# Performance work log

Measured on AMD Instinct MI355X. Metric: run time of the kernel, lower is better.

Reference implementation:

```python
import jax, jax.numpy as jnp
import numpy as np

N = 100000      # nodes
E = 1600000     # edges
IN_FEATS = 256
HID = 64
N_LAYERS = 3
OUT_FEATS = 32


def _glorot(key, shape):
    lim = np.sqrt(6.0 / (shape[0] + shape[1]))
    return jax.random.uniform(key, shape, jnp.float32, -lim, lim)


def setup_inputs() -> dict:
    key = jax.random.key(0)
    ks = jax.random.split(key, 8)
    feat = jax.random.normal(ks[0], (N, IN_FEATS), jnp.float32)
    src = jax.random.randint(ks[1], (E,), 0, N, jnp.int32)
    dst = jax.random.randint(ks[2], (E,), 0, N, jnp.int32)
    W1 = _glorot(ks[3], (IN_FEATS, HID)); b1 = jnp.zeros((HID,), jnp.float32)
    W2 = _glorot(ks[4], (HID, HID));      b2 = jnp.zeros((HID,), jnp.float32)
    W3 = _glorot(ks[5], (HID, HID));      b3 = jnp.zeros((HID,), jnp.float32)
    Wm = _glorot(ks[6], (HID * N_LAYERS, OUT_FEATS))
    bm = jnp.zeros((OUT_FEATS,), jnp.float32)
    return dict(feat=feat, src=src, dst=dst, W1=W1, b1=b1, W2=W2, b2=b2,
                W3=W3, b3=b3, Wm=Wm, bm=bm)


def _gcn_layer(feat, W, b, src, dst, do_isqrt, di_isqrt):
    # DGL GraphConv, norm='both', eval-mode dropout (identity), ReLU activation.
    # Weight applied before aggregation (mathematically identical, smaller SpMM).
    h = (feat * do_isqrt[:, None]) @ W            # [N, hid]
    agg = jax.ops.segment_sum(h[src], dst, num_segments=N)  # copy_u / sum
    return jax.nn.relu(agg * di_isqrt[:, None] + b)


def reference(feat, src, dst, W1, b1, W2, b2, W3, b3, Wm, bm):
    ones = jnp.ones((E,), jnp.float32)
    deg_out = jnp.clip(jax.ops.segment_sum(ones, src, num_segments=N), 1.0)
    deg_in = jnp.clip(jax.ops.segment_sum(ones, dst, num_segments=N), 1.0)
    do_isqrt = deg_out ** -0.5
    di_isqrt = deg_in ** -0.5

    h1 = _gcn_layer(feat, W1, b1, src, dst, do_isqrt, di_isqrt)
    h2 = _gcn_layer(h1, W2, b2, src, dst, do_isqrt, di_isqrt)
    h3 = _gcn_layer(h2, W3, b3, src, dst, do_isqrt, di_isqrt)

    # Jumping knowledge: mode='cat'
    h = jnp.concatenate([h1, h2, h3], axis=-1)    # [N, 192]
    # Final un-normalized message pass: copy_u / sum
    h = jax.ops.segment_sum(h[src], dst, num_segments=N)
    return h @ Wm + bm                            # [N, 32]
```

## Files before the change

### kernel.cpp

```cpp
#include <hip/hip_runtime.h>

#define IN_FEATS 256
#define HID 64
#define OUTF 32
#define JK (3*HID)

#define NB   256
#define BSH  9
#define NBLK 512

typedef __attribute__((ext_vector_type(4))) float floatx4;
typedef __attribute__((ext_vector_type(8))) short shortx8;

__device__ inline unsigned short f2bf(float f) {
    unsigned u = __float_as_uint(f);
    unsigned r = (u + 0x7fffu + ((u >> 16) & 1u)) >> 16;
    return (unsigned short)r;
}
__device__ inline float bf2f(unsigned short u) {
    return __uint_as_float(((unsigned)u) << 16);
}
__device__ inline unsigned pack2(float a, float b) {
    return (unsigned)f2bf(a) | ((unsigned)f2bf(b) << 16);
}
__device__ inline void acc8(uint4 u, float* a) {
    a[0] += bf2f((unsigned short)(u.x & 0xffff)); a[1] += bf2f((unsigned short)(u.x >> 16));
    a[2] += bf2f((unsigned short)(u.y & 0xffff)); a[3] += bf2f((unsigned short)(u.y >> 16));
    a[4] += bf2f((unsigned short)(u.z & 0xffff)); a[5] += bf2f((unsigned short)(u.z >> 16));
    a[6] += bf2f((unsigned short)(u.w & 0xffff)); a[7] += bf2f((unsigned short)(u.w >> 16));
}

__global__ __launch_bounds__(256) void p1_hist(const int* __restrict__ src,
                                               const int* __restrict__ dst, int E,
                                               int* __restrict__ bhd, int* __restrict__ bhs) {
    __shared__ int hd[NB], hs[NB];
    int b = blockIdx.x;
    for (int t = threadIdx.x; t < NB; t += 256) { hd[t] = 0; hs[t] = 0; }
    __syncthreads();
    int cb = (E + NBLK - 1) / NBLK;
    int beg = b * cb, end = min(beg + cb, E);
    for (int e = beg + threadIdx.x; e < end; e += 256) {
        atomicAdd(&hd[dst[e] >> BSH], 1);
        atomicAdd(&hs[src[e] >> BSH], 1);
    }
    __syncthreads();
    for (int t = threadIdx.x; t < NB; t += 256) {
        bhd[b * NB + t] = hd[t];
        bhs[b * NB + t] = hs[t];
    }
}

__global__ __launch_bounds__(256) void p2a_tot(const int* __restrict__ bhd,
                                               const int* __restrict__ bhs,
                                               int* __restrict__ totd, int* __restrict__ tots,
                                               int nblk,
                                               const float* __restrict__ W1, const float* __restrict__ W2,
                                               const float* __restrict__ W3, const float* __restrict__ Wm,
                                               unsigned short* __restrict__ W1t, unsigned short* __restrict__ W2t,
                                               unsigned short* __restrict__ W3t, unsigned short* __restrict__ Wmt) {
    if ((int)blockIdx.x >= 512) {
        int i = (blockIdx.x - 512) * 256 + threadIdx.x;
        if (i < 256 * 64) { int k = i / 64, c = i % 64; W1t[c * 256 + k] = f2bf(W1[i]); return; }
        int j = i - 256 * 64;
        if (j < 64 * 64) { int k = j / 64, c = j % 64; W2t[c * 64 + k] = f2bf(W2[j]); return; }
        int j2 = j - 64 * 64;
        if (j2 < 64 * 64) { int k = j2 / 64, c = j2 % 64; W3t[c * 64 + k] = f2bf(W3[j2]); return; }
        int j3 = j2 - 64 * 64;
        if (j3 < 192 * 32) { int k = j3 / 32, c = j3 % 32; Wmt[c * 192 + k] = f2bf(Wm[j3]); }
        return;
    }
    __shared__ int s[256];
    int side = blockIdx.x >> 8;
    int t = blockIdx.x & 255;
    const int* bh = side ? bhs : bhd;
    int acc = 0;
    for (int k = threadIdx.x; k < nblk; k += 256) acc += bh[k * NB + t];
    s[threadIdx.x] = acc;
    __syncthreads();
    for (int off = 128; off > 0; off >>= 1) {
        if (threadIdx.x < off) s[threadIdx.x] += s[threadIdx.x + off];
        __syncthreads();
    }
    if (threadIdx.x == 0) (side ? tots : totd)[t] = s[0];
}

__global__ __launch_bounds__(256) void p2b_scan(const int* __restrict__ totd,
                                                const int* __restrict__ tots,
                                                int* __restrict__ based, int* __restrict__ bases) {
    __shared__ int s[256];
    const int* tot = blockIdx.x ? tots : totd;
    int* bb = blockIdx.x ? bases : based;
    int t = threadIdx.x;
    int v = tot[t];
    s[t] = v;
    __syncthreads();
    for (int off = 1; off < 256; off <<= 1) {
        int u = (t >= off) ? s[t - off] : 0;
        __syncthreads();
        s[t] += u;
        __syncthreads();
    }
    bb[t] = s[t] - v;
    if (t == 255) bb[256] = s[255];
}

__global__ __launch_bounds__(256) void p2c_off(int* __restrict__ bhd, int* __restrict__ bhs,
                                               const int* __restrict__ based,
                                               const int* __restrict__ bases, int nblk) {
    __shared__ int s[256];
    int side = blockIdx.x >> 8;
    int t = blockIdx.x & 255;
    int* bh = side ? bhs : bhd;
    int carry = (side ? bases : based)[t];
    for (int k0 = 0; k0 < nblk; k0 += 256) {
        int k = k0 + threadIdx.x;
        int v = (k < nblk) ? bh[k * NB + t] : 0;
        s[threadIdx.x] = v;
        __syncthreads();
        for (int off = 1; off < 256; off <<= 1) {
            int u = (threadIdx.x >= off) ? s[threadIdx.x - off] : 0;
            __syncthreads();
            s[threadIdx.x] += u;
            __syncthreads();
        }
        if (k < nblk) bh[k * NB + t] = carry + s[threadIdx.x] - v;
        int tot = s[255];
        __syncthreads();
        carry += tot;
    }
}

__global__ __launch_bounds__(256) void p3m(
    const int* __restrict__ src, const int* __restrict__ dst, int E,
    const int* __restrict__ bhd, const int* __restrict__ bhs,
    int* __restrict__ pairbuf, int* __restrict__ srctmp,
    const float* __restrict__ feat, const unsigned short* __restrict__ W1t,
    unsigned short* __restrict__ outb, int nrows) {
    __shared__ int curd[NB], curs[NB];
    __shared__ unsigned short Al[64 * 64];
    __shared__ unsigned short Bl[64 * 64];

    if ((int)blockIdx.x < NBLK) {
        int b = blockIdx.x;
        for (int t = threadIdx.x; t < NB; t += 256) {
            curd[t] = bhd[b * NB + t];
            curs[t] = bhs[b * NB + t];
        }
        __syncthreads();
        int cb = (E + NBLK - 1) / NBLK;
        int beg = b * cb, end = min(beg + cb, E);
        for (int e = beg + threadIdx.x; e < end; e += 256) {
            int d = dst[e], sv = src[e];
            int pd = atomicAdd(&curd[d >> BSH], 1);
            pairbuf[pd] = ((d & 511) << 17) | sv;
            int ps = atomicAdd(&curs[sv >> BSH], 1);
            srctmp[ps] = sv;
        }
        return;
    }
    const int tid = threadIdx.x;
    const int wave = tid >> 6, lane = tid & 63;
    const int g = lane >> 4, lm = lane & 15;
    const int gr0 = (blockIdx.x - NBLK) * 64;

    floatx4 acc[4];
    #pragma unroll
    for (int f = 0; f < 4; ++f) acc[f] = (floatx4)0.f;

    for (int kc = 0; kc < IN_FEATS; kc += 64) {
        for (int c = tid; c < 64 * 8; c += 256) {
            int row = c >> 3, c8 = c & 7;
            int grow = gr0 + row;
            unsigned short v[8];
            if (grow < nrows) {
                const float* Xf = feat + (size_t)grow * IN_FEATS + kc + c8 * 8;
                #pragma unroll
                for (int j = 0; j < 8; ++j) v[j] = f2bf(Xf[j]);
            } else {
                #pragma unroll
                for (int j = 0; j < 8; ++j) v[j] = 0;
            }
            int off = (row * 64 + c8 * 8) ^ ((row & 7) << 3);
            *(uint4*)&Al[off] = *(uint4*)v;
        }
        for (int c = tid; c < 64 * 8; c += 256) {
            int col = c >> 3, c8 = c & 7;
            uint4 raw = *(const uint4*)&W1t[(size_t)col * IN_FEATS + kc + c8 * 8];
            int off = (col * 64 + c8 * 8) ^ ((col & 7) << 3);
            *(uint4*)&Bl[off] = raw;
        }
        __syncthreads();
        #pragma unroll
        for (int ks = 0; ks < 2; ++ks) {
            int arow = wave * 16 + lm;
            int aoff = (arow * 64 + ks * 32 + g * 8) ^ ((arow & 7) << 3);
            shortx8 afrag = *(shortx8*)&Al[aoff];
            #pragma unroll
            for (int f = 0; f < 4; ++f) {
                int col = f * 16 + lm;
                int boff = (col * 64 + ks * 32 + g * 8) ^ ((col & 7) << 3);
                shortx8 bfrag = *(shortx8*)&Bl[boff];
                acc[f] = __builtin_amdgcn_mfma_f32_16x16x32_bf16(afrag, bfrag, acc[f], 0, 0, 0);
            }
        }
        __syncthreads();
    }
    #pragma unroll
    for (int f = 0; f < 4; ++f) {
        #pragma unroll
        for (int r = 0; r < 4; ++r) {
            int grow = gr0 + wave * 16 + g * 4 + r;
            if (grow < nrows) outb[(size_t)grow * 64 + f * 16 + lm] = f2bf(acc[f][r]);
        }
    }
}

__global__ __launch_bounds__(256) void p4c(const int* __restrict__ pairbuf,
                                           const int* __restrict__ srctmp,
                                           const int* __restrict__ based,
                                           const int* __restrict__ bases,
                                           int* __restrict__ indptr, int* __restrict__ colbuf,
                                           float* __restrict__ di_isqrt, float* __restrict__ do_isqrt,
                                           int N, int E, int nbuck) {
    __shared__ int cnt[512], lp[512], s[256];
    int t = threadIdx.x;
    if ((int)blockIdx.x >= nbuck) {
        int b = blockIdx.x - nbuck;
        int nbase = b << BSH;
        int nn = min(512, N - nbase);
        cnt[t] = 0; cnt[t + 256] = 0;
        __syncthreads();
        int eb = bases[b], ee = bases[b + 1];
        for (int e = eb + t; e < ee; e += 256)
            atomicAdd(&cnt[srctmp[e] - nbase], 1);
        __syncthreads();
        for (int i = t; i < nn; i += 256)
            do_isqrt[nbase + i] = rsqrtf((float)max(cnt[i], 1));
        return;
    }
    int b = blockIdx.x;
    int nbase = b << BSH;
    int nn = min(512, N - nbase);
    cnt[t] = 0; cnt[t + 256] = 0;
    __syncthreads();
    int eb = based[b], ee = based[b + 1];
    for (int e = eb + t; e < ee; e += 256)
        atomicAdd(&cnt[pairbuf[e] >> 17], 1);
    __syncthreads();
    int a0 = cnt[2 * t], a1 = cnt[2 * t + 1];
    int psum = a0 + a1;
    s[t] = psum;
    __syncthreads();
    for (int off = 1; off < 256; off <<= 1) {
        int v = (t >= off) ? s[t - off] : 0;
        __syncthreads();
        s[t] += v;
        __syncthreads();
    }
    int ebase = s[t] - psum;
    lp[2 * t] = ebase;
    lp[2 * t + 1] = ebase + a0;
    __syncthreads();
    for (int i = t; i < nn; i += 256) {
        indptr[nbase + i] = eb + lp[i];
        di_isqrt[nbase + i] = rsqrtf((float)max(cnt[i], 1));
    }
    if (b == 0 && t == 0) indptr[N] = E;
    __syncthreads();
    for (int e = eb + t; e < ee; e += 256) {
        int pk = pairbuf[e];
        int pos = atomicAdd(&lp[pk >> 17], 1);
        colbuf[eb + pos] = pk & 0x1FFFF;
    }
}

__global__ __launch_bounds__(256) void scaleT(uint4* __restrict__ tmp,
                                              const float* __restrict__ dov, int N) {
    int j = threadIdx.x & 7;
    int node = blockIdx.x * 32 + (threadIdx.x >> 3);
    if (node >= N) return;
    float sc = dov[node];
    uint4 u = tmp[(size_t)node * 8 + j];
    uint4 o;
    o.x = pack2(bf2f((unsigned short)(u.x & 0xffff)) * sc, bf2f((unsigned short)(u.x >> 16)) * sc);
    o.y = pack2(bf2f((unsigned short)(u.y & 0xffff)) * sc, bf2f((unsigned short)(u.y >> 16)) * sc);
    o.z = pack2(bf2f((unsigned short)(u.z & 0xffff)) * sc, bf2f((unsigned short)(u.z >> 16)) * sc);
    o.w = pack2(bf2f((unsigned short)(u.w & 0xffff)) * sc, bf2f((unsigned short)(u.w >> 16)) * sc);
    tmp[(size_t)node * 8 + j] = o;
}

template <int COLS, int K>
__global__ __launch_bounds__(256) void mgemm(
    const unsigned short* __restrict__ X, int ldx,
    const unsigned short* __restrict__ Wt,
    const float* __restrict__ rs,
    unsigned short* __restrict__ out, int ldo, int nrows) {
    constexpr int KC = 64;
    constexpr int NFRAG = COLS / 16;
    __shared__ unsigned short Al[64 * KC];
    __shared__ unsigned short Bl[COLS * KC];

    const int tid = threadIdx.x;
    const int wave = tid >> 6, lane = tid & 63;
    const int g = lane >> 4, lm = lane & 15;
    const int gr0 = blockIdx.x * 64;

    floatx4 acc[NFRAG];
    #pragma unroll
    for (int f = 0; f < NFRAG; ++f) acc[f] = (floatx4)0.f;

    for (int kc = 0; kc < K; kc += KC) {
        for (int c = tid; c < 64 * 8; c += 256) {
            int row = c >> 3, c8 = c & 7;
            int grow = gr0 + row;
            unsigned short v[8];
            if (grow < nrows) {
                uint4 raw = *(const uint4*)(X + (size_t)grow * ldx + kc + c8 * 8);
                unsigned short* rp = (unsigned short*)&raw;
                if (rs) {
                    float sc = rs[grow];
                    #pragma unroll
                    for (int j = 0; j < 8; ++j) v[j] = f2bf(bf2f(rp[j]) * sc);
                } else {
                    #pragma unroll
                    for (int j = 0; j < 8; ++j) v[j] = rp[j];
                }
            } else {
                #pragma unroll
                for (int j = 0; j < 8; ++j) v[j] = 0;
            }
            int off = (row * KC + c8 * 8) ^ ((row & 7) << 3);
            *(uint4*)&Al[off] = *(uint4*)v;
        }
        for (int c = tid; c < COLS * 8; c += 256) {
            int col = c >> 3, c8 = c & 7;
            uint4 raw = *(const uint4*)&Wt[(size_t)col * K + kc + c8 * 8];
            int off = (col * KC + c8 * 8) ^ ((col & 7) << 3);
            *(uint4*)&Bl[off] = raw;
        }
        __syncthreads();
        #pragma unroll
        for (int ks = 0; ks < 2; ++ks) {
            int arow = wave * 16 + lm;
            int aoff = (arow * KC + ks * 32 + g * 8) ^ ((arow & 7) << 3);
            shortx8 afrag = *(shortx8*)&Al[aoff];
            #pragma unroll
            for (int f = 0; f < NFRAG; ++f) {
                int col = f * 16 + lm;
                int boff = (col * KC + ks * 32 + g * 8) ^ ((col & 7) << 3);
                shortx8 bfrag = *(shortx8*)&Bl[boff];
                acc[f] = __builtin_amdgcn_mfma_f32_16x16x32_bf16(afrag, bfrag, acc[f], 0, 0, 0);
            }
        }
        __syncthreads();
    }
    #pragma unroll
    for (int f = 0; f < NFRAG; ++f) {
        #pragma unroll
        for (int r = 0; r < 4; ++r) {
            int grow = gr0 + wave * 16 + g * 4 + r;
            if (grow < nrows) out[(size_t)grow * ldo + f * 16 + lm] = f2bf(acc[f][r]);
        }
    }
}

__global__ __launch_bounds__(256) void gatherH(
    const int* __restrict__ indptr, const int* __restrict__ colbuf,
    const uint4* __restrict__ fin,
    const float* __restrict__ di, const float* __restrict__ bias,
    uint4* __restrict__ hout, int ldh, int coff, int N) {
    int j = threadIdx.x & 7;
    int node = blockIdx.x * 32 + (threadIdx.x >> 3);
    if (node >= N) return;
    int beg = indptr[node], end = indptr[node + 1];
    float a[8] = {};
    int e = beg;
    for (; e + 4 <= end; e += 4) {
        int4 cc = *(const int4*)&colbuf[e];
        uint4 u0 = fin[(size_t)cc.x * 8 + j];
        uint4 u1 = fin[(size_t)cc.y * 8 + j];
        uint4 u2 = fin[(size_t)cc.z * 8 + j];
        uint4 u3 = fin[(size_t)cc.w * 8 + j];
        acc8(u0, a); acc8(u1, a); acc8(u2, a); acc8(u3, a);
    }
    for (; e < end; ++e) acc8(fin[(size_t)colbuf[e] * 8 + j], a);
    float dval = di[node];
    float4 b0 = *(const float4*)&bias[j * 8];
    float4 b1 = *(const float4*)&bias[j * 8 + 4];
    float r[8];
    r[0] = fmaxf(a[0] * dval + b0.x, 0.f); r[1] = fmaxf(a[1] * dval + b0.y, 0.f);
    r[2] = fmaxf(a[2] * dval + b0.z, 0.f); r[3] = fmaxf(a[3] * dval + b0.w, 0.f);
    r[4] = fmaxf(a[4] * dval + b1.x, 0.f); r[5] = fmaxf(a[5] * dval + b1.y, 0.f);
    r[6] = fmaxf(a[6] * dval + b1.z, 0.f); r[7] = fmaxf(a[7] * dval + b1.w, 0.f);
    uint4 o;
    o.x = pack2(r[0], r[1]); o.y = pack2(r[2], r[3]);
    o.z = pack2(r[4], r[5]); o.w = pack2(r[6], r[7]);
    hout[(size_t)node * ldh + coff + j] = o;
}

__global__ __launch_bounds__(256) void final_gather(
    const int* __restrict__ indptr, const int* __restrict__ colbuf,
    const uint4* __restrict__ P4,
    const float* __restrict__ bm,
    float* __restrict__ out, int N) {
    int j = threadIdx.x & 3;
    int node = blockIdx.x * 64 + (threadIdx.x >> 2);
    if (node >= N) return;
    int beg = indptr[node], end = indptr[node + 1];
    float a[8] = {};
    int e = beg;
    for (; e + 4 <= end; e += 4) {
        int4 cc = *(const int4*)&colbuf[e];
        uint4 u0 = P4[(size_t)cc.x * 4 + j];
        uint4 u1 = P4[(size_t)cc.y * 4 + j];
        uint4 u2 = P4[(size_t)cc.z * 4 + j];
        uint4 u3 = P4[(size_t)cc.w * 4 + j];
        acc8(u0, a); acc8(u1, a); acc8(u2, a); acc8(u3, a);
    }
    for (; e < end; ++e) acc8(P4[(size_t)colbuf[e] * 4 + j], a);
    float4 b0 = *(const float4*)&bm[j * 8];
    float4 b1 = *(const float4*)&bm[j * 8 + 4];
    float4 o0 = make_float4(a[0] + b0.x, a[1] + b0.y, a[2] + b0.z, a[3] + b0.w);
    float4 o1 = make_float4(a[4] + b1.x, a[5] + b1.y, a[6] + b1.z, a[7] + b1.w);
    *(float4*)&out[(size_t)node * 32 + j * 8] = o0;
    *(float4*)&out[(size_t)node * 32 + j * 8 + 4] = o1;
}

extern "C" void kernel_launch(void* const* d_in, const int* in_sizes, int n_in,
                              void* d_out, int out_size, void* d_ws, size_t ws_size,
                              hipStream_t stream) {
    const float* feat = (const float*)d_in[0];
    const int*   src  = (const int*)d_in[1];
    const int*   dst  = (const int*)d_in[2];
    const float* W1   = (const float*)d_in[3];
    const float* b1   = (const float*)d_in[4];
    const float* W2   = (const float*)d_in[5];
    const float* b2   = (const float*)d_in[6];
    const float* W3   = (const float*)d_in[7];
    const float* b3   = (const float*)d_in[8];
    const float* Wm   = (const float*)d_in[9];
    const float* bm   = (const float*)d_in[10];
    float* out = (float*)d_out;

    const int N = in_sizes[0] / IN_FEATS;
    const int E = in_sizes[1];
    const int NBUCK = (N + 511) >> BSH;

    char* wsp = (char*)d_ws;
    auto alloc = [&](size_t bytes) {
        void* p = (void*)wsp;
        wsp += ((bytes + 255) / 256) * 256;
        return p;
    };
    int*   indptr   = (int*)alloc((size_t)(N + 1) * 4);
    int*   colbuf   = (int*)alloc((size_t)E * 4);
    int*   bhd      = (int*)alloc((size_t)NBLK * NB * 4);
    int*   bhs      = (int*)alloc((size_t)NBLK * NB * 4);
    int*   totd     = (int*)alloc(256 * 4);
    int*   tots     = (int*)alloc(256 * 4);
    int*   based    = (int*)alloc(257 * 4);
    int*   bases    = (int*)alloc(257 * 4);
    float* do_isqrt = (float*)alloc((size_t)N * 4);
    float* di_isqrt = (float*)alloc((size_t)N * 4);
    unsigned short* W1t = (unsigned short*)alloc(256 * 64 * 2);
    unsigned short* W2t = (unsigned short*)alloc(64 * 64 * 2);
    unsigned short* W3t = (unsigned short*)alloc(64 * 64 * 2);
    unsigned short* Wmt = (unsigned short*)alloc(192 * 32 * 2);
    unsigned short* Hb  = (unsigned short*)alloc((size_t)N * JK * 2);
    int*   pairbuf  = (int*)alloc((size_t)E * 4);
    int*   srctmp   = (int*)alloc((size_t)E * 4);
    unsigned short* tmp = (unsigned short*)alloc((size_t)N * HID * 2);
    unsigned short* P   = (unsigned short*)alloc((size_t)N * OUTF * 2);

    const int GB = (N + 63) / 64;
    const int GGB = (N + 31) / 32;

    p1_hist<<<NBLK, 256, 0, stream>>>(src, dst, E, bhd, bhs);
    p2a_tot<<<512 + 120, 256, 0, stream>>>(bhd, bhs, totd, tots, NBLK,
                                           W1, W2, W3, Wm, W1t, W2t, W3t, Wmt);
    p2b_scan<<<2, 256, 0, stream>>>(totd, tots, based, bases);
    p2c_off<<<512, 256, 0, stream>>>(bhd, bhs, based, bases, NBLK);
    p3m<<<NBLK + GB, 256, 0, stream>>>(src, dst, E, bhd, bhs, pairbuf, srctmp,
                                       feat, W1t, tmp, N);
    p4c<<<2 * NBUCK, 256, 0, stream>>>(pairbuf, srctmp, based, bases, indptr, colbuf,
                                       di_isqrt, do_isqrt, N, E, NBUCK);
    scaleT<<<GGB, 256, 0, stream>>>((uint4*)tmp, do_isqrt, N);

    gatherH<<<GGB, 256, 0, stream>>>(indptr, colbuf, (const uint4*)tmp, di_isqrt, b1,
                                     (uint4*)Hb, 24, 0, N);
    mgemm<HID, HID><<<GB, 256, 0, stream>>>(Hb, JK, W2t, do_isqrt, tmp, HID, N);
    gatherH<<<GGB, 256, 0, stream>>>(indptr, colbuf, (const uint4*)tmp, di_isqrt, b2,
                                     (uint4*)Hb, 24, 8, N);
    mgemm<HID, HID><<<GB, 256, 0, stream>>>(Hb + HID, JK, W3t, do_isqrt, tmp, HID, N);
    gatherH<<<GGB, 256, 0, stream>>>(indptr, colbuf, (const uint4*)tmp, di_isqrt, b3,
                                     (uint4*)Hb, 24, 16, N);
    mgemm<OUTF, JK><<<GB, 256, 0, stream>>>(Hb, JK, Wmt, nullptr, P, OUTF, N);
    final_gather<<<(N + 63) / 64, 256, 0, stream>>>(indptr, colbuf, (const uint4*)P, bm, out, N);
}
```

Measured before the change: 244.6 us.

## Fold out-degree scaling into first gather, widen buckets, vectorize edge binning

Removes the scaleT pass by applying the out-degree normalization inside the first-layer gather, scaling each neighbor row while accumulating. The bucket sort now uses half as many, wider buckets (1024 nodes each) and half as many binning blocks. The histogram and scatter loops read edges with int4 loads. This saves one kernel launch and a full read-write of tmp, at the cost of an extra scalar load per edge in layer 1 and more per-block work and shared-memory atomics in the sort.

```diff
diff --git a/kernel.cpp b/kernel.cpp
--- a/kernel.cpp
+++ b/kernel.cpp
@@ -5,9 +5,9 @@
 #define OUTF 32
 #define JK (3*HID)
 
-#define NB   256
-#define BSH  9
-#define NBLK 512
+#define NB    128
+#define BSH   10
+#define NBLK2 256
 
 typedef __attribute__((ext_vector_type(4))) float floatx4;
 typedef __attribute__((ext_vector_type(8))) short shortx8;
@@ -28,6 +28,22 @@
     a[2] += bf2f((unsigned short)(u.y & 0xffff)); a[3] += bf2f((unsigned short)(u.y >> 16));
     a[4] += bf2f((unsigned short)(u.z & 0xffff)); a[5] += bf2f((unsigned short)(u.z >> 16));
     a[6] += bf2f((unsigned short)(u.w & 0xffff)); a[7] += bf2f((unsigned short)(u.w >> 16));
+}
+__device__ inline void acc8s(uint4 u, float* a, float s) {
+    a[0] = fmaf(bf2f((unsigned short)(u.x & 0xffff)), s, a[0]);
+    a[1] = fmaf(bf2f((unsigned short)(u.x >> 16)), s, a[1]);
+    a[2] = fmaf(bf2f((unsigned short)(u.y & 0xffff)), s, a[2]);
+    a[3] = fmaf(bf2f((unsigned short)(u.y >> 16)), s, a[3]);
+    a[4] = fmaf(bf2f((unsigned short)(u.z & 0xffff)), s, a[4]);
+    a[5] = fmaf(bf2f((unsigned short)(u.z >> 16)), s, a[5]);
+    a[6] = fmaf(bf2f((unsigned short)(u.w & 0xffff)), s, a[6]);
+    a[7] = fmaf(bf2f((unsigned short)(u.w >> 16)), s, a[7]);
+}
+
+__device__ inline void chunk_bounds(int E, int b, int& beg, int& end) {
+    int cb = ((E + NBLK2 - 1) / NBLK2 + 3) & ~3;
+    beg = b * cb;
+    end = min(beg + cb, E);
 }
 
 __global__ __launch_bounds__(256) void p1_hist(const int* __restrict__ src,
@@ -37,9 +53,18 @@
     int b = blockIdx.x;
     for (int t = threadIdx.x; t < NB; t += 256) { hd[t] = 0; hs[t] = 0; }
     __syncthreads();
-    int cb = (E + NBLK - 1) / NBLK;
-    int beg = b * cb, end = min(beg + cb, E);
-    for (int e = beg + threadIdx.x; e < end; e += 256) {
+    int beg, end;
+    chunk_bounds(E, b, beg, end);
+    int e = beg + threadIdx.x * 4;
+    for (; e + 4 <= end; e += 1024) {
+        int4 dd = *(const int4*)&dst[e];
+        int4 ss = *(const int4*)&src[e];
+        atomicAdd(&hd[dd.x >> BSH], 1); atomicAdd(&hd[dd.y >> BSH], 1);
+        atomicAdd(&hd[dd.z >> BSH], 1); atomicAdd(&hd[dd.w >> BSH], 1);
+        atomicAdd(&hs[ss.x >> BSH], 1); atomicAdd(&hs[ss.y >> BSH], 1);
+        atomicAdd(&hs[ss.z >> BSH], 1); atomicAdd(&hs[ss.w >> BSH], 1);
+    }
+    for (; e < end; ++e) {
         atomicAdd(&hd[dst[e] >> BSH], 1);
         atomicAdd(&hs[src[e] >> BSH], 1);
     }
@@ -58,8 +83,8 @@
                                                const float* __restrict__ W3, const float* __restrict__ Wm,
                                                unsigned short* __restrict__ W1t, unsigned short* __restrict__ W2t,
                                                unsigned short* __restrict__ W3t, unsigned short* __restrict__ Wmt) {
-    if ((int)blockIdx.x >= 512) {
-        int i = (blockIdx.x - 512) * 256 + threadIdx.x;
+    if ((int)blockIdx.x >= 2 * NB) {
+        int i = (blockIdx.x - 2 * NB) * 256 + threadIdx.x;
         if (i < 256 * 64) { int k = i / 64, c = i % 64; W1t[c * 256 + k] = f2bf(W1[i]); return; }
         int j = i - 256 * 64;
         if (j < 64 * 64) { int k = j / 64, c = j % 64; W2t[c * 64 + k] = f2bf(W2[j]); return; }
@@ -70,8 +95,8 @@
         return;
     }
     __shared__ int s[256];
-    int side = blockIdx.x >> 8;
-    int t = blockIdx.x & 255;
+    int side = blockIdx.x >> 7;
+    int t = blockIdx.x & (NB - 1);
     const int* bh = side ? bhs : bhd;
     int acc = 0;
     for (int k = threadIdx.x; k < nblk; k += 256) acc += bh[k * NB + t];
@@ -84,32 +109,32 @@
     if (threadIdx.x == 0) (side ? tots : totd)[t] = s[0];
 }
 
-__global__ __launch_bounds__(256) void p2b_scan(const int* __restrict__ totd,
+__global__ __launch_bounds__(128) void p2b_scan(const int* __restrict__ totd,
                                                 const int* __restrict__ tots,
                                                 int* __restrict__ based, int* __restrict__ bases) {
-    __shared__ int s[256];
+    __shared__ int s[NB];
     const int* tot = blockIdx.x ? tots : totd;
     int* bb = blockIdx.x ? bases : based;
     int t = threadIdx.x;
     int v = tot[t];
     s[t] = v;
     __syncthreads();
-    for (int off = 1; off < 256; off <<= 1) {
+    for (int off = 1; off < NB; off <<= 1) {
         int u = (t >= off) ? s[t - off] : 0;
         __syncthreads();
         s[t] += u;
         __syncthreads();
     }
     bb[t] = s[t] - v;
-    if (t == 255) bb[256] = s[255];
+    if (t == NB - 1) bb[NB] = s[NB - 1];
 }
 
 __global__ __launch_bounds__(256) void p2c_off(int* __restrict__ bhd, int* __restrict__ bhs,
                                                const int* __restrict__ based,
                                                const int* __restrict__ bases, int nblk) {
     __shared__ int s[256];
-    int side = blockIdx.x >> 8;
-    int t = blockIdx.x & 255;
+    int side = blockIdx.x >> 7;
+    int t = blockIdx.x & (NB - 1);
     int* bh = side ? bhs : bhd;
     int carry = (side ? bases : based)[t];
     for (int k0 = 0; k0 < nblk; k0 += 256) {
@@ -140,19 +165,32 @@
     __shared__ unsigned short Al[64 * 64];
     __shared__ unsigned short Bl[64 * 64];
 
-    if ((int)blockIdx.x < NBLK) {
+    if ((int)blockIdx.x < NBLK2) {
         int b = blockIdx.x;
         for (int t = threadIdx.x; t < NB; t += 256) {
             curd[t] = bhd[b * NB + t];
             curs[t] = bhs[b * NB + t];
         }
         __syncthreads();
-        int cb = (E + NBLK - 1) / NBLK;
-        int beg = b * cb, end = min(beg + cb, E);
-        for (int e = beg + threadIdx.x; e < end; e += 256) {
+        int beg, end;
+        chunk_bounds(E, b, beg, end);
+        int e = beg + threadIdx.x * 4;
+        for (; e + 4 <= end; e += 1024) {
+            int4 dd = *(const int4*)&dst[e];
+            int4 ss = *(const int4*)&src[e];
+            int p0 = atomicAdd(&curd[dd.x >> BSH], 1); pairbuf[p0] = ((dd.x & 1023) << 17) | ss.x;
+            int p1 = atomicAdd(&curd[dd.y >> BSH], 1); pairbuf[p1] = ((dd.y & 1023) << 17) | ss.y;
+            int p2 = atomicAdd(&curd[dd.z >> BSH], 1); pairbuf[p2] = ((dd.z & 1023) << 17) | ss.z;
+            int p3 = atomicAdd(&curd[dd.w >> BSH], 1); pairbuf[p3] = ((dd.w & 1023) << 17) | ss.w;
+            int q0 = atomicAdd(&curs[ss.x >> BSH], 1); srctmp[q0] = ss.x;
+            int q1 = atomicAdd(&curs[ss.y >> BSH], 1); srctmp[q1] = ss.y;
+            int q2 = atomicAdd(&curs[ss.z >> BSH], 1); srctmp[q2] = ss.z;
+            int q3 = atomicAdd(&curs[ss.w >> BSH], 1); srctmp[q3] = ss.w;
+        }
+        for (; e < end; ++e) {
             int d = dst[e], sv = src[e];
             int pd = atomicAdd(&curd[d >> BSH], 1);
-            pairbuf[pd] = ((d & 511) << 17) | sv;
+            pairbuf[pd] = ((d & 1023) << 17) | sv;
             int ps = atomicAdd(&curs[sv >> BSH], 1);
             srctmp[ps] = sv;
         }
@@ -161,7 +199,7 @@
     const int tid = threadIdx.x;
     const int wave = tid >> 6, lane = tid & 63;
     const int g = lane >> 4, lm = lane & 15;
-    const int gr0 = (blockIdx.x - NBLK) * 64;
+    const int gr0 = (blockIdx.x - NBLK2) * 64;
 
     floatx4 acc[4];
     #pragma unroll
@@ -222,13 +260,14 @@
                                            int* __restrict__ indptr, int* __restrict__ colbuf,
                                            float* __restrict__ di_isqrt, float* __restrict__ do_isqrt,
                                            int N, int E, int nbuck) {
-    __shared__ int cnt[512], lp[512], s[256];
+    __shared__ int cnt[1024], lp[1024], s[256];
     int t = threadIdx.x;
     if ((int)blockIdx.x >= nbuck) {
         int b = blockIdx.x - nbuck;
         int nbase = b << BSH;
-        int nn = min(512, N - nbase);
-        cnt[t] = 0; cnt[t + 256] = 0;
+        int nn = min(1024, N - nbase);
+        #pragma unroll
+        for (int i = 0; i < 4; ++i) cnt[t + 256 * i] = 0;
         __syncthreads();
         int eb = bases[b], ee = bases[b + 1];
         for (int e = eb + t; e < ee; e += 256)
@@ -240,15 +279,16 @@
     }
     int b = blockIdx.x;
     int nbase = b << BSH;
-    int nn = min(512, N - nbase);
-    cnt[t] = 0; cnt[t + 256] = 0;
+    int nn = min(1024, N - nbase);
+    #pragma unroll
+    for (int i = 0; i < 4; ++i) cnt[t + 256 * i] = 0;
     __syncthreads();
     int eb = based[b], ee = based[b + 1];
     for (int e = eb + t; e < ee; e += 256)
         atomicAdd(&cnt[pairbuf[e] >> 17], 1);
     __syncthreads();
-    int a0 = cnt[2 * t], a1 = cnt[2 * t + 1];
-    int psum = a0 + a1;
+    int c0 = cnt[4 * t], c1 = cnt[4 * t + 1], c2 = cnt[4 * t + 2], c3 = cnt[4 * t + 3];
+    int psum = c0 + c1 + c2 + c3;
     s[t] = psum;
     __syncthreads();
     for (int off = 1; off < 256; off <<= 1) {
@@ -257,9 +297,11 @@
         s[t] += v;
         __syncthreads();
     }
-    int ebase = s[t] - psum;
-    lp[2 * t] = ebase;
-    lp[2 * t + 1] = ebase + a0;
+    int base = s[t] - psum;
+    lp[4 * t] = base;
+    lp[4 * t + 1] = base + c0;
+    lp[4 * t + 2] = base + c0 + c1;
+    lp[4 * t + 3] = base + c0 + c1 + c2;
     __syncthreads();
     for (int i = t; i < nn; i += 256) {
         indptr[nbase + i] = eb + lp[i];
@@ -272,21 +314,6 @@
         int pos = atomicAdd(&lp[pk >> 17], 1);
         colbuf[eb + pos] = pk & 0x1FFFF;
     }
-}
-
-__global__ __launch_bounds__(256) void scaleT(uint4* __restrict__ tmp,
-                                              const float* __restrict__ dov, int N) {
-    int j = threadIdx.x & 7;
-    int node = blockIdx.x * 32 + (threadIdx.x >> 3);
-    if (node >= N) return;
-    float sc = dov[node];
-    uint4 u = tmp[(size_t)node * 8 + j];
-    uint4 o;
-    o.x = pack2(bf2f((unsigned short)(u.x & 0xffff)) * sc, bf2f((unsigned short)(u.x >> 16)) * sc);
-    o.y = pack2(bf2f((unsigned short)(u.y & 0xffff)) * sc, bf2f((unsigned short)(u.y >> 16)) * sc);
-    o.z = pack2(bf2f((unsigned short)(u.z & 0xffff)) * sc, bf2f((unsigned short)(u.z >> 16)) * sc);
-    o.w = pack2(bf2f((unsigned short)(u.w & 0xffff)) * sc, bf2f((unsigned short)(u.w >> 16)) * sc);
-    tmp[(size_t)node * 8 + j] = o;
 }
 
 template <int COLS, int K>
@@ -364,9 +391,11 @@
     }
 }
 
+template <bool DOV>
 __global__ __launch_bounds__(256) void gatherH(
     const int* __restrict__ indptr, const int* __restrict__ colbuf,
     const uint4* __restrict__ fin,
+    const float* __restrict__ dov,
     const float* __restrict__ di, const float* __restrict__ bias,
     uint4* __restrict__ hout, int ldh, int coff, int N) {
     int j = threadIdx.x & 7;
@@ -381,9 +410,18 @@
         uint4 u1 = fin[(size_t)cc.y * 8 + j];
         uint4 u2 = fin[(size_t)cc.z * 8 + j];
         uint4 u3 = fin[(size_t)cc.w * 8 + j];
-        acc8(u0, a); acc8(u1, a); acc8(u2, a); acc8(u3, a);
-    }
-    for (; e < end; ++e) acc8(fin[(size_t)colbuf[e] * 8 + j], a);
+        if (DOV) {
+            acc8s(u0, a, dov[cc.x]); acc8s(u1, a, dov[cc.y]);
+            acc8s(u2, a, dov[cc.z]); acc8s(u3, a, dov[cc.w]);
+        } else {
+            acc8(u0, a); acc8(u1, a); acc8(u2, a); acc8(u3, a);
+        }
+    }
+    for (; e < end; ++e) {
+        int c = colbuf[e];
+        uint4 u = fin[(size_t)c * 8 + j];
+        if (DOV) acc8s(u, a, dov[c]); else acc8(u, a);
+    }
     float dval = di[node];
     float4 b0 = *(const float4*)&bias[j * 8];
     float4 b1 = *(const float4*)&bias[j * 8 + 4];
@@ -444,7 +482,7 @@
 
     const int N = in_sizes[0] / IN_FEATS;
     const int E = in_sizes[1];
-    const int NBUCK = (N + 511) >> BSH;
+    const int NBUCK = (N + 1023) >> BSH;
 
     char* wsp = (char*)d_ws;
     auto alloc = [&](size_t bytes) {
@@ -454,12 +492,12 @@
     };
     int*   indptr   = (int*)alloc((size_t)(N + 1) * 4);
     int*   colbuf   = (int*)alloc((size_t)E * 4);
-    int*   bhd      = (int*)alloc((size_t)NBLK * NB * 4);
-    int*   bhs      = (int*)alloc((size_t)NBLK * NB * 4);
-    int*   totd     = (int*)alloc(256 * 4);
-    int*   tots     = (int*)alloc(256 * 4);
-    int*   based    = (int*)alloc(257 * 4);
-    int*   bases    = (int*)alloc(257 * 4);
+    int*   bhd      = (int*)alloc((size_t)NBLK2 * NB * 4);
+    int*   bhs      = (int*)alloc((size_t)NBLK2 * NB * 4);
+    int*   totd     = (int*)alloc(NB * 4);
+    int*   tots     = (int*)alloc(NB * 4);
+    int*   based    = (int*)alloc((NB + 1) * 4);
+    int*   bases    = (int*)alloc((NB + 1) * 4);
     float* do_isqrt = (float*)alloc((size_t)N * 4);
     float* di_isqrt = (float*)alloc((size_t)N * 4);
     unsigned short* W1t = (unsigned short*)alloc(256 * 64 * 2);
@@ -475,25 +513,24 @@
     const int GB = (N + 63) / 64;
     const int GGB = (N + 31) / 32;
 
-    p1_hist<<<NBLK, 256, 0, stream>>>(src, dst, E, bhd, bhs);
-    p2a_tot<<<512 + 120, 256, 0, stream>>>(bhd, bhs, totd, tots, NBLK,
-                                           W1, W2, W3, Wm, W1t, W2t, W3t, Wmt);
-    p2b_scan<<<2, 256, 0, stream>>>(totd, tots, based, bases);
-    p2c_off<<<512, 256, 0, stream>>>(bhd, bhs, based, bases, NBLK);
-    p3m<<<NBLK + GB, 256, 0, stream>>>(src, dst, E, bhd, bhs, pairbuf, srctmp,
-                                       feat, W1t, tmp, N);
+    p1_hist<<<NBLK2, 256, 0, stream>>>(src, dst, E, bhd, bhs);
+    p2a_tot<<<2 * NB + 120, 256, 0, stream>>>(bhd, bhs, totd, tots, NBLK2,
+                                              W1, W2, W3, Wm, W1t, W2t, W3t, Wmt);
+    p2b_scan<<<2, NB, 0, stream>>>(totd, tots, based, bases);
+    p2c_off<<<2 * NB, 256, 0, stream>>>(bhd, bhs, based, bases, NBLK2);
+    p3m<<<NBLK2 + GB, 256, 0, stream>>>(src, dst, E, bhd, bhs, pairbuf, srctmp,
+                                        feat, W1t, tmp, N);
     p4c<<<2 * NBUCK, 256, 0, stream>>>(pairbuf, srctmp, based, bases, indptr, colbuf,
                                        di_isqrt, do_isqrt, N, E, NBUCK);
-    scaleT<<<GGB, 256, 0, stream>>>((uint4*)tmp, do_isqrt, N);
-
-    gatherH<<<GGB, 256, 0, stream>>>(indptr, colbuf, (const uint4*)tmp, di_isqrt, b1,
-                                     (uint4*)Hb, 24, 0, N);
+
+    gatherH<true><<<GGB, 256, 0, stream>>>(indptr, colbuf, (const uint4*)tmp, do_isqrt,
+                                           di_isqrt, b1, (uint4*)Hb, 24, 0, N);
     mgemm<HID, HID><<<GB, 256, 0, stream>>>(Hb, JK, W2t, do_isqrt, tmp, HID, N);
-    gatherH<<<GGB, 256, 0, stream>>>(indptr, colbuf, (const uint4*)tmp, di_isqrt, b2,
-                                     (uint4*)Hb, 24, 8, N);
+    gatherH<false><<<GGB, 256, 0, stream>>>(indptr, colbuf, (const uint4*)tmp, nullptr,
+                                            di_isqrt, b2, (uint4*)Hb, 24, 8, N);
     mgemm<HID, HID><<<GB, 256, 0, stream>>>(Hb + HID, JK, W3t, do_isqrt, tmp, HID, N);
-    gatherH<<<GGB, 256, 0, stream>>>(indptr, colbuf, (const uint4*)tmp, di_isqrt, b3,
-                                     (uint4*)Hb, 24, 16, N);
+    gatherH<false><<<GGB, 256, 0, stream>>>(indptr, colbuf, (const uint4*)tmp, nullptr,
+                                            di_isqrt, b3, (uint4*)Hb, 24, 16, N);
     mgemm<OUTF, JK><<<GB, 256, 0, stream>>>(Hb, JK, Wmt, nullptr, P, OUTF, N);
     final_gather<<<(N + 63) / 64, 256, 0, stream>>>(indptr, colbuf, (const uint4*)P, bm, out, N);
 }
```

After: 236.0 us. 3.5% less time.
